# Performance work log

Hardware: AMD Instinct MI355X
Metric: run time of the kernel (lower is better)

The kernel has to match this reference:

```python
import jax, jax.numpy as jnp
import numpy as np


def setup_inputs() -> dict:
    key = jax.random.key(0)
    k1, k2, k3, k4, k5, k6 = jax.random.split(key, 6)
    B, C, H, W = 8, 128, 256, 256
    Ch = C // 2
    u = jax.random.normal(k1, (B, C, H, W), dtype=jnp.float32)
    weights_input = jax.random.normal(k2, (B, C, H, W), dtype=jnp.float32)
    # 1x1 conv params (stored as [out, in])
    w1 = jax.random.normal(k3, (Ch, C), dtype=jnp.float32) * (1.0 / np.sqrt(C))
    b1 = jax.random.normal(k4, (Ch,), dtype=jnp.float32) * 0.01
    w2 = jax.random.normal(k5, (4, Ch), dtype=jnp.float32) * (1.0 / np.sqrt(Ch))
    b2 = jax.random.normal(k6, (4,), dtype=jnp.float32) * 0.01
    return {"u": u, "weights_input": weights_input, "w1": w1, "b1": b1, "w2": w2, "b2": b2}


def _shift_up(u):  # neighbor above: zero-pad top row
    return jnp.pad(u[:, :, :-1, :], ((0, 0), (0, 0), (1, 0), (0, 0)))


def _shift_down(u):
    return jnp.pad(u[:, :, 1:, :], ((0, 0), (0, 0), (0, 1), (0, 0)))


def _shift_left(u):
    return jnp.pad(u[:, :, :, :-1], ((0, 0), (0, 0), (0, 0), (1, 0)))


def _shift_right(u):
    return jnp.pad(u[:, :, :, 1:], ((0, 0), (0, 0), (0, 0), (0, 1)))


def reference(u, weights_input, w1, b1, w2, b2):
    # weight_net: 1x1 conv -> ReLU -> 1x1 conv -> Softplus
    h = jax.nn.relu(jnp.einsum('bchw,oc->bohw', weights_input, w1) + b1[None, :, None, None])
    w = jax.nn.softplus(jnp.einsum('bchw,oc->bohw', h, w2) + b2[None, :, None, None])  # (B,4,H,W)
    w_up, w_down, w_left, w_right = w[:, 0:1], w[:, 1:2], w[:, 2:3], w[:, 3:4]
    lap = (w_up * (_shift_up(u) - u)
           + w_down * (_shift_down(u) - u)
           + w_left * (_shift_left(u) - u)
           + w_right * (_shift_right(u) - u))
    return lap
```

## Files before the change

### kernel.cpp

```cpp
#include <hip/hip_runtime.h>
#include <math.h>

constexpr int Bn = 8, Cn = 128, ChN = 64, Hn = 256, Wn = 256;
constexpr long long HWn  = (long long)Hn * Wn;
constexpr long long CHWn = (long long)Cn * HWn;

typedef short  s16x8  __attribute__((ext_vector_type(8)));
typedef __bf16 bf16x8 __attribute__((ext_vector_type(8)));
typedef float  f32x4  __attribute__((ext_vector_type(4)));

static __device__ __forceinline__ unsigned short f2bf(float f) {
    union { float f; unsigned u; } v; v.f = f;
    unsigned r = (v.u + 0x7FFFu + ((v.u >> 16) & 1u)) >> 16;
    return (unsigned short)r;
}
static __device__ __forceinline__ bf16x8 tobf(s16x8 s) {
    bf16x8 r; __builtin_memcpy(&r, &s, 16); return r;
}

__global__ void prep(const float* __restrict__ w1, const float* __restrict__ w2,
                     uint4* __restrict__ af, float* __restrict__ w2t) {
    int idx = blockIdx.x * 256 + threadIdx.x;
    if (idx < 1024) {
        int lane = idx & 63, kb = (idx >> 6) & 3, ot = idx >> 8;
        int row   = ot * 16 + (lane & 15);
        int kbase = kb * 32 + ((lane >> 4) & 3) * 8;
        const float* src = w1 + row * Cn + kbase;
        unsigned short b[8];
        #pragma unroll
        for (int t = 0; t < 8; ++t) b[t] = f2bf(src[t]);
        uint4 r;
        r.x = (unsigned)b[0] | ((unsigned)b[1] << 16);
        r.y = (unsigned)b[2] | ((unsigned)b[3] << 16);
        r.z = (unsigned)b[4] | ((unsigned)b[5] << 16);
        r.w = (unsigned)b[6] | ((unsigned)b[7] << 16);
        af[idx] = r;
    } else if (idx < 1024 + ChN * 4) {
        int t = idx - 1024;
        w2t[t] = w2[(t & 3) * ChN + (t >> 2)];
    }
}

__device__ __forceinline__ float softplus_f(float x) {
    return fmaxf(x, 0.0f) + log1pf(expf(-fabsf(x)));
}

__global__ __launch_bounds__(256) void wfield(
    const float* __restrict__ wi,
    const uint4* __restrict__ af,
    const float* __restrict__ w2t,
    const float* __restrict__ b1,
    const float* __restrict__ b2,
    float* __restrict__ wpk)
{
    const int tid  = threadIdx.x;
    const int wv   = tid >> 6;
    const int lane = tid & 63;
    const int l15  = lane & 15;
    const int lg   = lane >> 4;

    const int wid = blockIdx.x * 4 + wv;

    for (int q = 0; q < 2; ++q) {
        const int chunk = wid * 2 + q;
        const int p0    = chunk * 16;
        const int bb    = p0 >> 16;
        const int rem   = p0 & (int)(HWn - 1);

        const float* wip = wi + (size_t)bb * CHWn + rem + l15;

        float xb[32];
        #pragma unroll
        for (int kb = 0; kb < 4; ++kb)
            #pragma unroll
            for (int t = 0; t < 8; ++t)
                xb[kb * 8 + t] = wip[(size_t)(kb * 32 + lg * 8 + t) * HWn];

        f32x4 acc[4];
        #pragma unroll
        for (int ot = 0; ot < 4; ++ot)
            acc[ot] = *(const f32x4*)(b1 + ot * 16 + lg * 4);

        #pragma unroll
        for (int kb = 0; kb < 4; ++kb) {
            s16x8 bs;
            #pragma unroll
            for (int t = 0; t < 8; ++t) bs[t] = (short)f2bf(xb[kb * 8 + t]);
            bf16x8 bfrag = tobf(bs);
            #pragma unroll
            for (int ot = 0; ot < 4; ++ot) {
                s16x8 as = ((const s16x8*)af)[(ot * 4 + kb) * 64 + lane];
                acc[ot] = __builtin_amdgcn_mfma_f32_16x16x32_bf16(
                              tobf(as), bfrag, acc[ot], 0, 0, 0);
            }
        }

        float a0 = 0.f, a1 = 0.f, a2 = 0.f, a3 = 0.f;
        #pragma unroll
        for (int ot = 0; ot < 4; ++ot) {
            #pragma unroll
            for (int r = 0; r < 4; ++r) {
                int o = ot * 16 + lg * 4 + r;
                float hv = fmaxf(acc[ot][r], 0.f);
                const float4 w4v = ((const float4*)w2t)[o];
                a0 = fmaf(w4v.x, hv, a0);
                a1 = fmaf(w4v.y, hv, a1);
                a2 = fmaf(w4v.z, hv, a2);
                a3 = fmaf(w4v.w, hv, a3);
            }
        }
        a0 += __shfl_xor(a0, 16); a0 += __shfl_xor(a0, 32);
        a1 += __shfl_xor(a1, 16); a1 += __shfl_xor(a1, 32);
        a2 += __shfl_xor(a2, 16); a2 += __shfl_xor(a2, 32);
        a3 += __shfl_xor(a3, 16); a3 += __shfl_xor(a3, 32);

        if (lg == 0) {
            const int px = p0 + l15;
            const int i  = (px >> 8) & 255;
            const int j  = px & 255;
            float* wrow = wpk + ((size_t)(bb * Hn + i) * 4) * Wn + j;
            wrow[0 * Wn] = softplus_f(a0 + b2[0]);
            wrow[1 * Wn] = softplus_f(a1 + b2[1]);
            wrow[2 * Wn] = softplus_f(a2 + b2[2]);
            wrow[3 * Wn] = softplus_f(a3 + b2[3]);
        }
    }
}

__global__ __launch_bounds__(256) void stencil5(
    const float* __restrict__ u,
    const float* __restrict__ wpk,
    float* __restrict__ out)
{
    const int bb    = blockIdx.x & 7;
    const int rest  = blockIdx.x >> 3;
    const int strip = rest & 31;
    const int cq    = rest >> 5;
    const int tid   = threadIdx.x;
    const int wv    = tid >> 6;
    const int lane  = tid & 63;

    const int i0 = strip * 8;
    const int c0 = cq * 32 + wv * 8;
    const int j4 = lane * 4;

    __shared__ float wlds[8 * 4 * 256];

    const float* wsrc = wpk + ((size_t)(bb * Hn + i0) * 4) * Wn;
    #pragma unroll
    for (int k = 0; k < 8; ++k) {
        f32x4 v = *(const f32x4*)(wsrc + (size_t)(k * 256 + tid) * 4);
        *(f32x4*)(wlds + (k * 256 + tid) * 4) = v;
    }
    __syncthreads();

    const float4 z4 = {0.f, 0.f, 0.f, 0.f};

    #pragma unroll 2
    for (int cc = 0; cc < 8; ++cc) {
        const int c = c0 + cc;
        const size_t plane = ((size_t)bb * Cn + c) * HWn;
        const float* up0 = u   + plane + j4;
        float*       po  = out + plane + j4;

        float4 R[10];
        #pragma unroll
        for (int k = 0; k < 10; ++k) {
            const int i = i0 - 1 + k;
            R[k] = (i >= 0 && i < Hn) ? *(const float4*)(up0 + (size_t)i * Wn) : z4;
        }

        #pragma unroll
        for (int r = 0; r < 8; ++r) {
            float4 ctr = R[r + 1], up4 = R[r], dn4 = R[r + 2];
            const f32x4* wrow = (const f32x4*)(wlds + (size_t)(r * 4) * 256);
            f32x4 WU = wrow[0 * 64 + lane];
            f32x4 WD = wrow[1 * 64 + lane];
            f32x4 WL = wrow[2 * 64 + lane];
            f32x4 WR = wrow[3 * 64 + lane];

            float lw = __shfl(ctr.w, lane - 1);
            float rw = __shfl(ctr.x, lane + 1);
            float lfx = (lane == 0)  ? 0.f : lw;
            float rtw = (lane == 63) ? 0.f : rw;

            f32x4 WS = (WU + WD) + (WL + WR);

            f32x4 res;
            res[0] = fmaf(WU[0], up4.x, fmaf(WD[0], dn4.x, fmaf(WL[0], lfx,   fmaf(WR[0], ctr.y, -WS[0] * ctr.x))));
            res[1] = fmaf(WU[1], up4.y, fmaf(WD[1], dn4.y, fmaf(WL[1], ctr.x, fmaf(WR[1], ctr.z, -WS[1] * ctr.y))));
            res[2] = fmaf(WU[2], up4.z, fmaf(WD[2], dn4.z, fmaf(WL[2], ctr.y, fmaf(WR[2], ctr.w, -WS[2] * ctr.z))));
            res[3] = fmaf(WU[3], up4.w, fmaf(WD[3], dn4.w, fmaf(WL[3], ctr.z, fmaf(WR[3], rtw,   -WS[3] * ctr.w))));

            *(f32x4*)(po + (size_t)(i0 + r) * Wn) = res;
        }
    }
}

extern "C" void kernel_launch(void* const* d_in, const int* in_sizes, int n_in,
                              void* d_out, int out_size, void* d_ws, size_t ws_size,
                              hipStream_t stream) {
    const float* u  = (const float*)d_in[0];
    const float* wi = (const float*)d_in[1];
    const float* w1 = (const float*)d_in[2];
    const float* b1 = (const float*)d_in[3];
    const float* w2 = (const float*)d_in[4];
    const float* b2 = (const float*)d_in[5];
    float* out = (float*)d_out;

    uint4* af  = (uint4*)d_ws;
    float* w2t = (float*)((char*)d_ws + 16384);
    float* wpk = (float*)((char*)d_ws + 17408);

    prep<<<5, 256, 0, stream>>>(w1, w2, af, w2t);
    wfield<<<4096, 256, 0, stream>>>(wi, af, w2t, b1, b2, wpk);
    stencil5<<<1024, 256, 0, stream>>>(u, wpk, out);
}
```

Baseline: 190.5 us.

## Fuse weight-field MLP and stencil into one strip kernel via LDS

Result: slower. 437.9 us (+129.8%).

```diff
diff --git a/kernel.cpp b/kernel.cpp
--- a/kernel.cpp
+++ b/kernel.cpp
@@ -45,29 +45,33 @@
     return fmaxf(x, 0.0f) + log1pf(expf(-fabsf(x)));
 }
 
-__global__ __launch_bounds__(256) void wfield(
+__global__ __launch_bounds__(1024, 1) void fused_strip(
+    const float* __restrict__ u,
     const float* __restrict__ wi,
     const uint4* __restrict__ af,
     const float* __restrict__ w2t,
     const float* __restrict__ b1,
     const float* __restrict__ b2,
-    float* __restrict__ wpk)
+    float* __restrict__ out)
 {
-    const int tid  = threadIdx.x;
-    const int wv   = tid >> 6;
-    const int lane = tid & 63;
-    const int l15  = lane & 15;
-    const int lg   = lane >> 4;
+    const int tid   = threadIdx.x;
+    const int wv    = tid >> 6;
+    const int lane  = tid & 63;
+    const int l15   = lane & 15;
+    const int lg    = lane >> 4;
 
-    const int wid = blockIdx.x * 4 + wv;
+    const int bb    = blockIdx.x & 7;
+    const int strip = blockIdx.x >> 3;
+    const int i0    = strip * 8;
 
-    for (int q = 0; q < 2; ++q) {
-        const int chunk = wid * 2 + q;
-        const int p0    = chunk * 16;
-        const int bb    = p0 >> 16;
-        const int rem   = p0 & (int)(HWn - 1);
+    __shared__ float wlds[8 * 4 * 256];
 
-        const float* wip = wi + (size_t)bb * CHWn + rem + l15;
+    const size_t wibase = (size_t)bb * CHWn + (size_t)i0 * Wn;
+    #pragma unroll 2
+    for (int q = 0; q < 8; ++q) {
+        const int ch    = wv * 8 + q;
+        const int s_off = ch * 16 + l15;
+        const float* wip = wi + wibase + ch * 16 + l15;
 
         float xb[32];
         #pragma unroll
@@ -115,50 +119,24 @@
         a3 += __shfl_xor(a3, 16); a3 += __shfl_xor(a3, 32);
 
         if (lg == 0) {
-            const int px = p0 + l15;
-            const int i  = (px >> 8) & 255;
-            const int j  = px & 255;
-            float* wrow = wpk + ((size_t)(bb * Hn + i) * 4) * Wn + j;
-            wrow[0 * Wn] = softplus_f(a0 + b2[0]);
-            wrow[1 * Wn] = softplus_f(a1 + b2[1]);
-            wrow[2 * Wn] = softplus_f(a2 + b2[2]);
-            wrow[3 * Wn] = softplus_f(a3 + b2[3]);
+            const int r = s_off >> 8;
+            const int j = s_off & 255;
+            float* wrow = wlds + (r * 4) * 256 + j;
+            wrow[0 * 256] = softplus_f(a0 + b2[0]);
+            wrow[1 * 256] = softplus_f(a1 + b2[1]);
+            wrow[2 * 256] = softplus_f(a2 + b2[2]);
+            wrow[3 * 256] = softplus_f(a3 + b2[3]);
         }
     }
-}
 
-__global__ __launch_bounds__(256) void stencil5(
-    const float* __restrict__ u,
-    const float* __restrict__ wpk,
-    float* __restrict__ out)
-{
-    const int bb    = blockIdx.x & 7;
-    const int rest  = blockIdx.x >> 3;
-    const int strip = rest & 31;
-    const int cq    = rest >> 5;
-    const int tid   = threadIdx.x;
-    const int wv    = tid >> 6;
-    const int lane  = tid & 63;
-
-    const int i0 = strip * 8;
-    const int c0 = cq * 32 + wv * 8;
-    const int j4 = lane * 4;
-
-    __shared__ float wlds[8 * 4 * 256];
-
-    const float* wsrc = wpk + ((size_t)(bb * Hn + i0) * 4) * Wn;
-    #pragma unroll
-    for (int k = 0; k < 8; ++k) {
-        f32x4 v = *(const f32x4*)(wsrc + (size_t)(k * 256 + tid) * 4);
-        *(f32x4*)(wlds + (k * 256 + tid) * 4) = v;
-    }
     __syncthreads();
 
+    const int j4 = lane * 4;
     const float4 z4 = {0.f, 0.f, 0.f, 0.f};
 
     #pragma unroll 2
     for (int cc = 0; cc < 8; ++cc) {
-        const int c = c0 + cc;
+        const int c = wv * 8 + cc;
         const size_t plane = ((size_t)bb * Cn + c) * HWn;
         const float* up0 = u   + plane + j4;
         float*       po  = out + plane + j4;
@@ -173,7 +151,7 @@
         #pragma unroll
         for (int r = 0; r < 8; ++r) {
             float4 ctr = R[r + 1], up4 = R[r], dn4 = R[r + 2];
-            const f32x4* wrow = (const f32x4*)(wlds + (size_t)(r * 4) * 256);
+            const f32x4* wrow = (const f32x4*)(wlds + (r * 4) * 256);
             f32x4 WU = wrow[0 * 64 + lane];
             f32x4 WD = wrow[1 * 64 + lane];
             f32x4 WL = wrow[2 * 64 + lane];
@@ -210,9 +188,7 @@
 
     uint4* af  = (uint4*)d_ws;
     float* w2t = (float*)((char*)d_ws + 16384);
-    float* wpk = (float*)((char*)d_ws + 17408);
 
     prep<<<5, 256, 0, stream>>>(w1, w2, af, w2t);
-    wfield<<<4096, 256, 0, stream>>>(wi, af, w2t, b1, b2, wpk);
-    stencil5<<<1024, 256, 0, stream>>>(u, wpk, out);
+    fused_strip<<<256, 1024, 0, stream>>>(u, wi, af, w2t, b1, b2, out);
 }
```
